# Optimization experiments

Measured on AMD Instinct MI355X. Metric: run time of the kernel, lower is better.

The kernel has to match this reference:

```python
import jax, jax.numpy as jnp
import numpy as np

QUERY_DIM = 1024
KEY_DIM = 1024
NUM_HEADS = 16
HEAD_DIM = QUERY_DIM // NUM_HEADS


def setup_inputs() -> dict:
    key = jax.random.key(0)
    ks = jax.random.split(key, 11)
    B, Sq, Sk = 2, 2048, 2048
    s = 0.02
    return {
        "q": jax.random.normal(ks[0], (B, Sq, QUERY_DIM), jnp.float32),
        "k": jax.random.normal(ks[1], (B, Sk, KEY_DIM), jnp.float32),
        "v": jax.random.normal(ks[2], (B, Sk, KEY_DIM), jnp.float32),
        "Wq": jax.random.normal(ks[3], (QUERY_DIM, QUERY_DIM), jnp.float32) * s,
        "bq": jnp.zeros((QUERY_DIM,), jnp.float32),
        "Wk": jax.random.normal(ks[4], (KEY_DIM, QUERY_DIM), jnp.float32) * s,
        "bk": jnp.zeros((QUERY_DIM,), jnp.float32),
        "Wv": jax.random.normal(ks[5], (KEY_DIM, QUERY_DIM), jnp.float32) * s,
        "bv": jnp.zeros((QUERY_DIM,), jnp.float32),
        "Wo": jax.random.normal(ks[6], (QUERY_DIM, QUERY_DIM), jnp.float32) * s,
        "bo": jnp.zeros((QUERY_DIM,), jnp.float32),
    }


def reference(q, k, v, Wq, bq, Wk, bk, Wv, bv, Wo, bo):
    B, Sq, _ = q.shape
    Sk = k.shape[1]
    scale = HEAD_DIM ** -0.5
    # projections -> [B, H, S, Dh]
    qh = (q @ Wq + bq).reshape(B, Sq, NUM_HEADS, HEAD_DIM).transpose(0, 2, 1, 3)
    kh = (k @ Wk + bk).reshape(B, Sk, NUM_HEADS, HEAD_DIM).transpose(0, 2, 1, 3)
    vh = (v @ Wv + bv).reshape(B, Sk, NUM_HEADS, HEAD_DIM).transpose(0, 2, 1, 3)
    scores = jnp.einsum("bhqd,bhkd->bhqk", qh, kh) * scale
    attn = jax.nn.softmax(scores, axis=-1)
    out = jnp.einsum("bhqk,bhkd->bhqd", attn, vh)
    out = out.transpose(0, 2, 1, 3).reshape(B, Sq, QUERY_DIM)
    return out @ Wo + bo  # dropout is identity at inference
```

## Files before the change

### kernel.cpp

```cpp
#include <hip/hip_runtime.h>
#include <hip/hip_fp16.h>
#include <cstddef>


#define B_   2
#define S_   2048
#define D_   1024
#define H_   16
#define DH_  64

typedef _Float16 half8 __attribute__((ext_vector_type(8)));
typedef _Float16 half4 __attribute__((ext_vector_type(4)));
typedef float floatx4 __attribute__((ext_vector_type(4)));

#define MFMA32(a, b, c) __builtin_amdgcn_mfma_f32_16x16x32_f16((a), (b), (c), 0, 0, 0)
#define MFMA16(a, b, c) __builtin_amdgcn_mfma_f32_16x16x16f16((a), (b), (c), 0, 0, 0)

__global__ __launch_bounds__(256) void cvt3(
    const float* __restrict__ q, const float* __restrict__ k,
    const float* __restrict__ v,
    __half* __restrict__ qf, __half* __restrict__ kf, __half* __restrict__ vf)
{
    const float* srcs[3] = {q, k, v};
    __half* dsts[3] = {qf, kf, vf};
    const int z = blockIdx.y;
    const int i = blockIdx.x * 256 + threadIdx.x;
    const float4* s = (const float4*)srcs[z];
    const float4 a = s[2 * i], b = s[2 * i + 1];
    half8 h;
    h[0] = (_Float16)a.x; h[1] = (_Float16)a.y; h[2] = (_Float16)a.z; h[3] = (_Float16)a.w;
    h[4] = (_Float16)b.x; h[5] = (_Float16)b.y; h[6] = (_Float16)b.z; h[7] = (_Float16)b.w;
    *(half8*)&dsts[z][(size_t)i * 8] = h;
}

__global__ __launch_bounds__(256) void wtrans4(
    const float* __restrict__ Wq, const float* __restrict__ Wk,
    const float* __restrict__ Wv, const float* __restrict__ Wo,
    __half* __restrict__ Wtq, __half* __restrict__ Wtk,
    __half* __restrict__ Wtv, __half* __restrict__ Wto)
{
    __shared__ __align__(16) __half T[64][72];
    const float* Ws[4] = {Wq, Wk, Wv, Wo};
    __half* Wts[4] = {Wtq, Wtk, Wtv, Wto};
    const float* W = Ws[blockIdx.z];
    __half* Wt = Wts[blockIdx.z];
    const int tid = threadIdx.x;
    const int n0 = blockIdx.x * 64, k0 = blockIdx.y * 64;
    #pragma unroll
    for (int p = 0; p < 4; ++p) {
        const int c = tid + p * 256;
        const int kr = c >> 4, nc = (c & 15) * 4;
        const float4 a = *(const float4*)&W[(size_t)(k0 + kr) * D_ + n0 + nc];
        T[nc + 0][kr] = __float2half(a.x);
        T[nc + 1][kr] = __float2half(a.y);
        T[nc + 2][kr] = __float2half(a.z);
        T[nc + 3][kr] = __float2half(a.w);
    }
    __syncthreads();
    #pragma unroll
    for (int p = 0; p < 2; ++p) {
        const int c = tid + p * 256;
        const int nr = c >> 3, kc = (c & 7) * 8;
        *(half8*)&Wt[(size_t)(n0 + nr) * D_ + k0 + kc] = *(const half8*)&T[nr][kc];
    }
}

__device__ __forceinline__ void gemm_core(
    const __half* __restrict__ A, const __half* __restrict__ Bt,
    const float* __restrict__ bias, void* __restrict__ dst,
    const int mode, const float oscale)
{
    __shared__ __align__(16) char gsm[36864];
    __half (*As)[72] = (__half(*)[72])gsm;
    __half (*Bs)[72] = (__half(*)[72])(gsm + 18432);

    const int tid = threadIdx.x;
    const int m0 = blockIdx.y * 128, n0 = blockIdx.x * 128;
    const int lane = tid & 63, wv = tid >> 6;
    const int quad = lane >> 4, lr = lane & 15;
    const int wm0 = (wv >> 1) * 64, wn0 = (wv & 1) * 64;

    floatx4 acc[4][4];
    #pragma unroll
    for (int i = 0; i < 4; ++i)
        #pragma unroll
        for (int j = 0; j < 4; ++j)
            acc[i][j] = (floatx4){0.f, 0.f, 0.f, 0.f};

    half8 pa[4], pb[4];
    #pragma unroll
    for (int p = 0; p < 4; ++p) {
        const int c = tid + p * 256;
        const int row = c >> 3, seg = (c & 7) * 8;
        pa[p] = *(const half8*)&A [(size_t)(m0 + row) * D_ + seg];
        pb[p] = *(const half8*)&Bt[(size_t)(n0 + row) * D_ + seg];
    }

    for (int k0 = 0; k0 < D_; k0 += 64) {
        __syncthreads();
        #pragma unroll
        for (int p = 0; p < 4; ++p) {
            const int c = tid + p * 256;
            const int row = c >> 3, seg = (c & 7) * 8;
            *(half8*)&As[row][seg] = pa[p];
            *(half8*)&Bs[row][seg] = pb[p];
        }
        if (k0 + 64 < D_) {
            #pragma unroll
            for (int p = 0; p < 4; ++p) {
                const int c = tid + p * 256;
                const int row = c >> 3, seg = (c & 7) * 8;
                pa[p] = *(const half8*)&A [(size_t)(m0 + row) * D_ + k0 + 64 + seg];
                pb[p] = *(const half8*)&Bt[(size_t)(n0 + row) * D_ + k0 + 64 + seg];
            }
        }
        __syncthreads();
        #pragma unroll
        for (int ks = 0; ks < 2; ++ks) {
            const int ko = quad * 8 + ks * 32;
            half8 af[4], bf[4];
            #pragma unroll
            for (int i = 0; i < 4; ++i) af[i] = *(const half8*)&As[wm0 + i * 16 + lr][ko];
            #pragma unroll
            for (int j = 0; j < 4; ++j) bf[j] = *(const half8*)&Bs[wn0 + j * 16 + lr][ko];
            #pragma unroll
            for (int i = 0; i < 4; ++i)
                #pragma unroll
                for (int j = 0; j < 4; ++j)
                    acc[i][j] = MFMA32(af[i], bf[j], acc[i][j]);
        }
    }

    if (mode == 1) {
        float* out = (float*)dst;
        #pragma unroll
        for (int i = 0; i < 4; ++i) {
            #pragma unroll
            for (int j = 0; j < 4; ++j) {
                const int col = n0 + wn0 + j * 16 + lr;
                const float bval = bias[col];
                #pragma unroll
                for (int r = 0; r < 4; ++r) {
                    const int m = m0 + wm0 + i * 16 + quad * 4 + r;
                    out[(size_t)m * D_ + col] = acc[i][j][r] + bval;
                }
            }
        }
        return;
    }

    __syncthreads();
    __half (*Ct)[136] = (__half(*)[136])gsm;
    #pragma unroll
    for (int i = 0; i < 4; ++i) {
        #pragma unroll
        for (int j = 0; j < 4; ++j) {
            const int nl = wn0 + j * 16 + lr;
            const float bval = bias[n0 + nl];
            #pragma unroll
            for (int r = 0; r < 4; ++r) {
                const int ml = wm0 + i * 16 + quad * 4 + r;
                const _Float16 hv = (_Float16)((acc[i][j][r] + bval) * oscale);
                if (mode == 0) Ct[ml][nl] = hv;
                else           Ct[nl][ml] = hv;
            }
        }
    }
    __syncthreads();
    __half* oh = (__half*)dst;
    #pragma unroll
    for (int p = 0; p < 8; ++p) {
        const int row = (tid >> 4) + p * 16;
        const int cs  = (tid & 15) * 8;
        const half8 vls = *(const half8*)&Ct[row][cs];
        if (mode == 0) {
            const int m = m0 + row, col = n0 + cs;
            const int b = m >> 11, s = m & (S_ - 1);
            const int h = col >> 6, d = col & 63;
            *(half8*)&oh[(((size_t)(b * H_ + h) * S_ + s) << 6) + d] = vls;
        } else {
            const int col = n0 + row, m = m0 + cs;
            const int b = m >> 11, s = m & (S_ - 1);
            const int h = col >> 6, d = col & 63;
            *(half8*)&oh[((size_t)(b * H_ + h) * DH_ + d) * S_ + s] = vls;
        }
    }
}

__global__ __launch_bounds__(256) void gemm_proj(
    const __half* __restrict__ qf, const __half* __restrict__ kf,
    const __half* __restrict__ vf,
    const __half* __restrict__ Wtq, const __half* __restrict__ Wtk,
    const __half* __restrict__ Wtv,
    const float* __restrict__ bq, const float* __restrict__ bk,
    const float* __restrict__ bv,
    __half* __restrict__ qhf, __half* __restrict__ khf, __half* __restrict__ vht)
{
    const __half* As[3] = {qf, kf, vf};
    const __half* Bts[3] = {Wtq, Wtk, Wtv};
    const float* bs[3] = {bq, bk, bv};
    __half* ds[3] = {qhf, khf, vht};
    const int z = blockIdx.z;
    gemm_core(As[z], Bts[z], bs[z], ds[z], z == 2 ? 2 : 0,
              z == 0 ? 0.1803368801111244f : 1.0f);
}

__global__ __launch_bounds__(256) void gemm_final(
    const __half* __restrict__ attf, const __half* __restrict__ Wto,
    const float* __restrict__ bo, float* __restrict__ out)
{
    gemm_core(attf, Wto, bo, out, 1, 1.0f);
}

__global__ __launch_bounds__(256) void attn_f16(
    const __half* __restrict__ qhf, const __half* __restrict__ khf,
    const __half* __restrict__ vht, __half* __restrict__ attf)
{
    __shared__ __align__(16) char smem[31232];
    __half (*Qs)[72] = (__half(*)[72])smem;
    __half (*Ks)[72] = (__half(*)[72])(smem + 9216);
    __half (*Vs)[72] = (__half(*)[72])(smem + 18432);

    const int tid = threadIdx.x;
    const int lane = tid & 63, wv = tid >> 6;
    const int quad = lane >> 4, lr = lane & 15;
    const int bh = blockIdx.y;
    const int q0 = blockIdx.x * 64;
    const size_t hbase = (size_t)bh * S_ * DH_;

    #pragma unroll
    for (int p = 0; p < 2; ++p) {
        const int c = tid + p * 256;
        const int row = c >> 3, seg = (c & 7) * 8;
        *(half8*)&Qs[row][seg] = *(const half8*)&qhf[hbase + (size_t)(q0 + row) * DH_ + seg];
    }
    __syncthreads();
    half8 qB[4][2];
    #pragma unroll
    for (int qs = 0; qs < 4; ++qs)
        #pragma unroll
        for (int ks = 0; ks < 2; ++ks)
            qB[qs][ks] = *(const half8*)&Qs[qs * 16 + lr][quad * 8 + ks * 32];

    float lp[4] = {0.f, 0.f, 0.f, 0.f};
    floatx4 O[4][4];
    #pragma unroll
    for (int i = 0; i < 4; ++i)
        #pragma unroll
        for (int j = 0; j < 4; ++j)
            O[i][j] = (floatx4){0.f, 0.f, 0.f, 0.f};

    half8 pk[2], pv[2];
    #pragma unroll
    for (int p = 0; p < 2; ++p) {
        const int c = tid + p * 256;
        const int row = c >> 3, seg = (c & 7) * 8;
        pk[p] = *(const half8*)&khf[hbase + (size_t)row * DH_ + seg];
        pv[p] = *(const half8*)&vht[hbase + (size_t)row * S_ + seg];
    }

    for (int kt = 0; kt < S_; kt += 64) {
        __syncthreads();
        #pragma unroll
        for (int p = 0; p < 2; ++p) {
            const int c = tid + p * 256;
            const int row = c >> 3, seg = (c & 7) * 8;
            *(half8*)&Ks[row][seg] = pk[p];
            *(half8*)&Vs[row][seg] = pv[p];
        }
        if (kt + 64 < S_) {
            #pragma unroll
            for (int p = 0; p < 2; ++p) {
                const int c = tid + p * 256;
                const int row = c >> 3, seg = (c & 7) * 8;
                pk[p] = *(const half8*)&khf[hbase + (size_t)(kt + 64 + row) * DH_ + seg];
                pv[p] = *(const half8*)&vht[hbase + (size_t)row * S_ + kt + 64 + seg];
            }
        }
        __syncthreads();

        floatx4 s4[4];
        #pragma unroll
        for (int qs = 0; qs < 4; ++qs) s4[qs] = (floatx4){0.f, 0.f, 0.f, 0.f};
        #pragma unroll
        for (int ks = 0; ks < 2; ++ks) {
            const half8 aK = *(const half8*)&Ks[wv * 16 + lr][quad * 8 + ks * 32];
            #pragma unroll
            for (int qs = 0; qs < 4; ++qs)
                s4[qs] = MFMA32(aK, qB[qs][ks], s4[qs]);
        }

        half4 pB[4];
        #pragma unroll
        for (int qs = 0; qs < 4; ++qs) {
            #pragma unroll
            for (int r = 0; r < 4; ++r) {
                const float p = __builtin_amdgcn_exp2f(s4[qs][r]);
                lp[qs] += p;
                pB[qs][r] = (_Float16)p;
            }
        }

        #pragma unroll
        for (int ds = 0; ds < 4; ++ds) {
            const half4 aV = *(const half4*)&Vs[ds * 16 + lr][wv * 16 + quad * 4];
            #pragma unroll
            for (int qs = 0; qs < 4; ++qs)
                O[ds][qs] = MFMA16(aV, pB[qs], O[ds][qs]);
        }
    }

    __syncthreads();
    float* L    = (float*)(smem + 17408);
    float* invL = (float*)(smem + 21504);
    float (*R)[68] = (float(*)[68])smem;
    __half (*F)[72] = (__half(*)[72])(smem + 22016);

    #pragma unroll
    for (int qs = 0; qs < 4; ++qs)
        L[(wv * 4 + quad) * 64 + qs * 16 + lr] = lp[qs];
    __syncthreads();
    if (tid < 64) {
        float s = 0.f;
        #pragma unroll
        for (int i = 0; i < 16; ++i) s += L[i * 64 + tid];
        invL[tid] = 1.0f / s;
    }
    __syncthreads();

    const int qc = tid & 63, dg = tid >> 6;
    const float il = invL[qc];

    #pragma unroll
    for (int ds = 0; ds < 4; ++ds) {
        __syncthreads();
        #pragma unroll
        for (int qs = 0; qs < 4; ++qs)
            #pragma unroll
            for (int r = 0; r < 4; ++r)
                R[wv * 16 + quad * 4 + r][qs * 16 + lr] = O[ds][qs][r];
        __syncthreads();
        half4 hv;
        #pragma unroll
        for (int rr = 0; rr < 4; ++rr) {
            const int row = dg * 4 + rr;
            const float v = R[row][qc] + R[16 + row][qc] + R[32 + row][qc] + R[48 + row][qc];
            hv[rr] = (_Float16)(v * il);
        }
        *(half4*)&F[qc][ds * 16 + dg * 4] = hv;
    }
    __syncthreads();

    const int b = bh >> 4, h = bh & 15;
    const int qrow = tid >> 2, dseg = (tid & 3) * 16;
    __half* dstp = &attf[(((size_t)(b * S_ + q0 + qrow)) << 10) + h * DH_ + dseg];
    *(half8*)&dstp[0] = *(const half8*)&F[qrow][dseg];
    *(half8*)&dstp[8] = *(const half8*)&F[qrow][dseg + 8];
}

extern "C" void kernel_launch(void* const* d_in, const int* in_sizes, int n_in,
                              void* d_out, int out_size, void* d_ws, size_t ws_size,
                              hipStream_t stream) {
    const float* q  = (const float*)d_in[0];
    const float* k  = (const float*)d_in[1];
    const float* v  = (const float*)d_in[2];
    const float* Wq = (const float*)d_in[3];
    const float* bq = (const float*)d_in[4];
    const float* Wk = (const float*)d_in[5];
    const float* bk = (const float*)d_in[6];
    const float* Wv = (const float*)d_in[7];
    const float* bv = (const float*)d_in[8];
    const float* Wo = (const float*)d_in[9];
    const float* bo = (const float*)d_in[10];
    float* out = (float*)d_out;

    __half* ws = (__half*)d_ws;
    const size_t NE = (size_t)B_ * S_ * D_;
    __half* qf   = ws;
    __half* kf   = ws + NE;
    __half* vf   = ws + 2 * NE;
    __half* qhf  = ws + 3 * NE;
    __half* khf  = ws + 4 * NE;
    __half* vht  = ws + 5 * NE;
    __half* attf = ws + 6 * NE;
    __half* Wtq  = ws + 7 * NE;
    __half* Wtk  = Wtq + (size_t)D_ * D_;
    __half* Wtv  = Wtk + (size_t)D_ * D_;
    __half* Wto  = Wtv + (size_t)D_ * D_;

    const dim3 blk(256);
    cvt3<<<dim3((unsigned)(NE / 8 / 256), 3), blk, 0, stream>>>(q, k, v, qf, kf, vf);
    wtrans4<<<dim3(16, 16, 4), blk, 0, stream>>>(Wq, Wk, Wv, Wo, Wtq, Wtk, Wtv, Wto);

    gemm_proj<<<dim3(D_ / 128, (B_ * S_) / 128, 3), blk, 0, stream>>>(
        qf, kf, vf, Wtq, Wtk, Wtv, bq, bk, bv, qhf, khf, vht);

    attn_f16<<<dim3(S_ / 64, B_ * H_), blk, 0, stream>>>(qhf, khf, vht, attf);

    gemm_final<<<dim3(D_ / 128, (B_ * S_) / 128), blk, 0, stream>>>(attf, Wto, bo, out);
}
```

Baseline: 232.5 us.

## Load K/V fragments directly into registers in attention; merge prep kernels

The attention loop stops staging K and V tiles through shared memory. Each lane now loads its MFMA operand fragments straight from global memory, with the next K fragment prefetched into registers, which removes the per-tile LDS writes and both block barriers. Separately, the fp16 conversion and weight-transpose kernels are merged into one launch with a flat grid to cut launch overhead. The cost is that each lane issues narrower, less coalesced global loads (the V loads are 8-byte strided rows), and there is no shared reuse across waves, so more L2 traffic is risked.

```diff
diff --git a/kernel.cpp b/kernel.cpp
--- a/kernel.cpp
+++ b/kernel.cpp
@@ -16,36 +16,38 @@
 #define MFMA32(a, b, c) __builtin_amdgcn_mfma_f32_16x16x32_f16((a), (b), (c), 0, 0, 0)
 #define MFMA16(a, b, c) __builtin_amdgcn_mfma_f32_16x16x16f16((a), (b), (c), 0, 0, 0)
 
-__global__ __launch_bounds__(256) void cvt3(
+__global__ __launch_bounds__(256) void prep(
     const float* __restrict__ q, const float* __restrict__ k,
     const float* __restrict__ v,
-    __half* __restrict__ qf, __half* __restrict__ kf, __half* __restrict__ vf)
-{
-    const float* srcs[3] = {q, k, v};
-    __half* dsts[3] = {qf, kf, vf};
-    const int z = blockIdx.y;
-    const int i = blockIdx.x * 256 + threadIdx.x;
-    const float4* s = (const float4*)srcs[z];
-    const float4 a = s[2 * i], b = s[2 * i + 1];
-    half8 h;
-    h[0] = (_Float16)a.x; h[1] = (_Float16)a.y; h[2] = (_Float16)a.z; h[3] = (_Float16)a.w;
-    h[4] = (_Float16)b.x; h[5] = (_Float16)b.y; h[6] = (_Float16)b.z; h[7] = (_Float16)b.w;
-    *(half8*)&dsts[z][(size_t)i * 8] = h;
-}
-
-__global__ __launch_bounds__(256) void wtrans4(
+    __half* __restrict__ qf, __half* __restrict__ kf, __half* __restrict__ vf,
     const float* __restrict__ Wq, const float* __restrict__ Wk,
     const float* __restrict__ Wv, const float* __restrict__ Wo,
     __half* __restrict__ Wtq, __half* __restrict__ Wtk,
     __half* __restrict__ Wtv, __half* __restrict__ Wto)
 {
     __shared__ __align__(16) __half T[64][72];
+    const int tid = threadIdx.x;
+    const int bz = blockIdx.x;
+    if (bz < 6144) {
+        const float* srcs[3] = {q, k, v};
+        __half* dsts[3] = {qf, kf, vf};
+        const int z = bz >> 11;
+        const int i = (bz & 2047) * 256 + tid;
+        const float4* s = (const float4*)srcs[z];
+        const float4 a = s[2 * i], b = s[2 * i + 1];
+        half8 h;
+        h[0] = (_Float16)a.x; h[1] = (_Float16)a.y; h[2] = (_Float16)a.z; h[3] = (_Float16)a.w;
+        h[4] = (_Float16)b.x; h[5] = (_Float16)b.y; h[6] = (_Float16)b.z; h[7] = (_Float16)b.w;
+        *(half8*)&dsts[z][(size_t)i * 8] = h;
+        return;
+    }
+    const int idx = bz - 6144;
     const float* Ws[4] = {Wq, Wk, Wv, Wo};
     __half* Wts[4] = {Wtq, Wtk, Wtv, Wto};
-    const float* W = Ws[blockIdx.z];
-    __half* Wt = Wts[blockIdx.z];
-    const int tid = threadIdx.x;
-    const int n0 = blockIdx.x * 64, k0 = blockIdx.y * 64;
+    const float* W = Ws[idx >> 8];
+    __half* Wt = Wts[idx >> 8];
+    const int r = idx & 255;
+    const int n0 = (r & 15) * 64, k0 = (r >> 4) * 64;
     #pragma unroll
     for (int p = 0; p < 4; ++p) {
         const int c = tid + p * 256;
@@ -218,8 +220,6 @@
 {
     __shared__ __align__(16) char smem[31232];
     __half (*Qs)[72] = (__half(*)[72])smem;
-    __half (*Ks)[72] = (__half(*)[72])(smem + 9216);
-    __half (*Vs)[72] = (__half(*)[72])(smem + 18432);
 
     const int tid = threadIdx.x;
     const int lane = tid & 63, wv = tid >> 6;
@@ -241,6 +241,7 @@
         #pragma unroll
         for (int ks = 0; ks < 2; ++ks)
             qB[qs][ks] = *(const half8*)&Qs[qs * 16 + lr][quad * 8 + ks * 32];
+    __syncthreads();
 
     float lp[4] = {0.f, 0.f, 0.f, 0.f};
     floatx4 O[4][4];
@@ -250,45 +251,32 @@
         for (int j = 0; j < 4; ++j)
             O[i][j] = (floatx4){0.f, 0.f, 0.f, 0.f};
 
-    half8 pk[2], pv[2];
-    #pragma unroll
-    for (int p = 0; p < 2; ++p) {
-        const int c = tid + p * 256;
-        const int row = c >> 3, seg = (c & 7) * 8;
-        pk[p] = *(const half8*)&khf[hbase + (size_t)row * DH_ + seg];
-        pv[p] = *(const half8*)&vht[hbase + (size_t)row * S_ + seg];
-    }
+    const __half* kp = khf + hbase + (size_t)(wv * 16 + lr) * DH_ + quad * 8;
+    const __half* vp = vht + hbase + (size_t)lr * S_ + wv * 16 + quad * 4;
+
+    half8 cK0 = *(const half8*)(kp);
+    half8 cK1 = *(const half8*)(kp + 32);
 
     for (int kt = 0; kt < S_; kt += 64) {
-        __syncthreads();
-        #pragma unroll
-        for (int p = 0; p < 2; ++p) {
-            const int c = tid + p * 256;
-            const int row = c >> 3, seg = (c & 7) * 8;
-            *(half8*)&Ks[row][seg] = pk[p];
-            *(half8*)&Vs[row][seg] = pv[p];
-        }
+        half4 cV[4];
+        #pragma unroll
+        for (int ds = 0; ds < 4; ++ds)
+            cV[ds] = *(const half4*)(vp + (size_t)ds * 16 * S_ + kt);
+
+        half8 nK0, nK1;
         if (kt + 64 < S_) {
-            #pragma unroll
-            for (int p = 0; p < 2; ++p) {
-                const int c = tid + p * 256;
-                const int row = c >> 3, seg = (c & 7) * 8;
-                pk[p] = *(const half8*)&khf[hbase + (size_t)(kt + 64 + row) * DH_ + seg];
-                pv[p] = *(const half8*)&vht[hbase + (size_t)row * S_ + kt + 64 + seg];
-            }
-        }
-        __syncthreads();
+            const __half* kn = kp + (size_t)(kt + 64) * DH_;
+            nK0 = *(const half8*)(kn);
+            nK1 = *(const half8*)(kn + 32);
+        }
 
         floatx4 s4[4];
         #pragma unroll
         for (int qs = 0; qs < 4; ++qs) s4[qs] = (floatx4){0.f, 0.f, 0.f, 0.f};
         #pragma unroll
-        for (int ks = 0; ks < 2; ++ks) {
-            const half8 aK = *(const half8*)&Ks[wv * 16 + lr][quad * 8 + ks * 32];
-            #pragma unroll
-            for (int qs = 0; qs < 4; ++qs)
-                s4[qs] = MFMA32(aK, qB[qs][ks], s4[qs]);
-        }
+        for (int qs = 0; qs < 4; ++qs) s4[qs] = MFMA32(cK0, qB[qs][0], s4[qs]);
+        #pragma unroll
+        for (int qs = 0; qs < 4; ++qs) s4[qs] = MFMA32(cK1, qB[qs][1], s4[qs]);
 
         half4 pB[4];
         #pragma unroll
@@ -303,14 +291,14 @@
 
         #pragma unroll
         for (int ds = 0; ds < 4; ++ds) {
-            const half4 aV = *(const half4*)&Vs[ds * 16 + lr][wv * 16 + quad * 4];
             #pragma unroll
             for (int qs = 0; qs < 4; ++qs)
-                O[ds][qs] = MFMA16(aV, pB[qs], O[ds][qs]);
-        }
-    }
-
-    __syncthreads();
+                O[ds][qs] = MFMA16(cV[ds], pB[qs], O[ds][qs]);
+        }
+
+        cK0 = nK0; cK1 = nK1;
+    }
+
     float* L    = (float*)(smem + 17408);
     float* invL = (float*)(smem + 21504);
     float (*R)[68] = (float(*)[68])smem;
@@ -389,8 +377,8 @@
     __half* Wto  = Wtv + (size_t)D_ * D_;
 
     const dim3 blk(256);
-    cvt3<<<dim3((unsigned)(NE / 8 / 256), 3), blk, 0, stream>>>(q, k, v, qf, kf, vf);
-    wtrans4<<<dim3(16, 16, 4), blk, 0, stream>>>(Wq, Wk, Wv, Wo, Wtq, Wtk, Wtv, Wto);
+    prep<<<dim3(7168), blk, 0, stream>>>(q, k, v, qf, kf, vf,
+                                         Wq, Wk, Wv, Wo, Wtq, Wtk, Wtv, Wto);
 
     gemm_proj<<<dim3(D_ / 128, (B_ * S_) / 128, 3), blk, 0, stream>>>(
         qf, kf, vf, Wtq, Wtk, Wtv, bq, bk, bv, qhf, khf, vht);
```

Result: slower. 294.9 us (+26.9%).

## Swizzle GEMM block order and widen attention key tiles to 128

Applied to the files above, without the earlier changes.

Adds a grouped block-index swizzle to the projection and output GEMMs so neighbouring blocks share A/B tiles in cache. The attention kernel now processes 128 keys per iteration instead of 64, with each wave handling two 16-key groups. This halves the number of barrier-synchronised load/compute iterations and the per-tile overhead. The cost is more shared memory, with the K buffer aliased onto the Q staging area, which needs an extra sync, plus more prefetch registers.

```diff
diff --git a/kernel.cpp b/kernel.cpp
--- a/kernel.cpp
+++ b/kernel.cpp
@@ -68,14 +68,13 @@
 __device__ __forceinline__ void gemm_core(
     const __half* __restrict__ A, const __half* __restrict__ Bt,
     const float* __restrict__ bias, void* __restrict__ dst,
-    const int mode, const float oscale)
+    const int mode, const float oscale, const int m0, const int n0)
 {
     __shared__ __align__(16) char gsm[36864];
     __half (*As)[72] = (__half(*)[72])gsm;
     __half (*Bs)[72] = (__half(*)[72])(gsm + 18432);
 
     const int tid = threadIdx.x;
-    const int m0 = blockIdx.y * 128, n0 = blockIdx.x * 128;
     const int lane = tid & 63, wv = tid >> 6;
     const int quad = lane >> 4, lr = lane & 15;
     const int wm0 = (wv >> 1) * 64, wn0 = (wv & 1) * 64;
@@ -187,6 +186,13 @@
     }
 }
 
+__device__ __forceinline__ void swizzle_mn(int& m0, int& n0) {
+    const int id = blockIdx.y * gridDim.x + blockIdx.x;
+    const int grp = id >> 5, within = id & 31;
+    m0 = (grp * 4 + (within & 3)) * 128;
+    n0 = (within >> 2) * 128;
+}
+
 __global__ __launch_bounds__(256) void gemm_proj(
     const __half* __restrict__ qf, const __half* __restrict__ kf,
     const __half* __restrict__ vf,
@@ -201,25 +207,27 @@
     const float* bs[3] = {bq, bk, bv};
     __half* ds[3] = {qhf, khf, vht};
     const int z = blockIdx.z;
+    int m0, n0; swizzle_mn(m0, n0);
     gemm_core(As[z], Bts[z], bs[z], ds[z], z == 2 ? 2 : 0,
-              z == 0 ? 0.1803368801111244f : 1.0f);
+              z == 0 ? 0.1803368801111244f : 1.0f, m0, n0);
 }
 
 __global__ __launch_bounds__(256) void gemm_final(
     const __half* __restrict__ attf, const __half* __restrict__ Wto,
     const float* __restrict__ bo, float* __restrict__ out)
 {
-    gemm_core(attf, Wto, bo, out, 1, 1.0f);
+    int m0, n0; swizzle_mn(m0, n0);
+    gemm_core(attf, Wto, bo, out, 1, 1.0f, m0, n0);
 }
 
 __global__ __launch_bounds__(256) void attn_f16(
     const __half* __restrict__ qhf, const __half* __restrict__ khf,
     const __half* __restrict__ vht, __half* __restrict__ attf)
 {
-    __shared__ __align__(16) char smem[31232];
-    __half (*Qs)[72] = (__half(*)[72])smem;
-    __half (*Ks)[72] = (__half(*)[72])(smem + 9216);
-    __half (*Vs)[72] = (__half(*)[72])(smem + 18432);
+    __shared__ __align__(16) char smem[35840];
+    __half (*Ks)[72]  = (__half(*)[72])smem;
+    __half (*Vs)[136] = (__half(*)[136])(smem + 18432);
+    __half (*Qs)[72]  = (__half(*)[72])smem;
 
     const int tid = threadIdx.x;
     const int lane = tid & 63, wv = tid >> 6;
@@ -241,6 +249,7 @@
         #pragma unroll
         for (int ks = 0; ks < 2; ++ks)
             qB[qs][ks] = *(const half8*)&Qs[qs * 16 + lr][quad * 8 + ks * 32];
+    __syncthreads();
 
     float lp[4] = {0.f, 0.f, 0.f, 0.f};
     floatx4 O[4][4];
@@ -250,63 +259,70 @@
         for (int j = 0; j < 4; ++j)
             O[i][j] = (floatx4){0.f, 0.f, 0.f, 0.f};
 
-    half8 pk[2], pv[2];
-    #pragma unroll
-    for (int p = 0; p < 2; ++p) {
+    half8 pk[4], pv[4];
+    #pragma unroll
+    for (int p = 0; p < 4; ++p) {
         const int c = tid + p * 256;
-        const int row = c >> 3, seg = (c & 7) * 8;
-        pk[p] = *(const half8*)&khf[hbase + (size_t)row * DH_ + seg];
-        pv[p] = *(const half8*)&vht[hbase + (size_t)row * S_ + seg];
-    }
-
-    for (int kt = 0; kt < S_; kt += 64) {
-        __syncthreads();
-        #pragma unroll
-        for (int p = 0; p < 2; ++p) {
+        const int krow = c >> 3, kseg = (c & 7) * 8;
+        const int vrow = c >> 4, vseg = (c & 15) * 8;
+        pk[p] = *(const half8*)&khf[hbase + (size_t)krow * DH_ + kseg];
+        pv[p] = *(const half8*)&vht[hbase + (size_t)vrow * S_ + vseg];
+    }
+
+    for (int kt = 0; kt < S_; kt += 128) {
+        __syncthreads();
+        #pragma unroll
+        for (int p = 0; p < 4; ++p) {
             const int c = tid + p * 256;
-            const int row = c >> 3, seg = (c & 7) * 8;
-            *(half8*)&Ks[row][seg] = pk[p];
-            *(half8*)&Vs[row][seg] = pv[p];
-        }
-        if (kt + 64 < S_) {
-            #pragma unroll
-            for (int p = 0; p < 2; ++p) {
+            const int krow = c >> 3, kseg = (c & 7) * 8;
+            const int vrow = c >> 4, vseg = (c & 15) * 8;
+            *(half8*)&Ks[krow][kseg] = pk[p];
+            *(half8*)&Vs[vrow][vseg] = pv[p];
+        }
+        if (kt + 128 < S_) {
+            #pragma unroll
+            for (int p = 0; p < 4; ++p) {
                 const int c = tid + p * 256;
-                const int row = c >> 3, seg = (c & 7) * 8;
-                pk[p] = *(const half8*)&khf[hbase + (size_t)(kt + 64 + row) * DH_ + seg];
-                pv[p] = *(const half8*)&vht[hbase + (size_t)row * S_ + kt + 64 + seg];
-            }
-        }
-        __syncthreads();
-
-        floatx4 s4[4];
-        #pragma unroll
-        for (int qs = 0; qs < 4; ++qs) s4[qs] = (floatx4){0.f, 0.f, 0.f, 0.f};
-        #pragma unroll
-        for (int ks = 0; ks < 2; ++ks) {
-            const half8 aK = *(const half8*)&Ks[wv * 16 + lr][quad * 8 + ks * 32];
-            #pragma unroll
-            for (int qs = 0; qs < 4; ++qs)
-                s4[qs] = MFMA32(aK, qB[qs][ks], s4[qs]);
-        }
-
-        half4 pB[4];
-        #pragma unroll
-        for (int qs = 0; qs < 4; ++qs) {
-            #pragma unroll
-            for (int r = 0; r < 4; ++r) {
-                const float p = __builtin_amdgcn_exp2f(s4[qs][r]);
-                lp[qs] += p;
-                pB[qs][r] = (_Float16)p;
-            }
-        }
-
-        #pragma unroll
-        for (int ds = 0; ds < 4; ++ds) {
-            const half4 aV = *(const half4*)&Vs[ds * 16 + lr][wv * 16 + quad * 4];
-            #pragma unroll
-            for (int qs = 0; qs < 4; ++qs)
-                O[ds][qs] = MFMA16(aV, pB[qs], O[ds][qs]);
+                const int krow = c >> 3, kseg = (c & 7) * 8;
+                const int vrow = c >> 4, vseg = (c & 15) * 8;
+                pk[p] = *(const half8*)&khf[hbase + (size_t)(kt + 128 + krow) * DH_ + kseg];
+                pv[p] = *(const half8*)&vht[hbase + (size_t)vrow * S_ + kt + 128 + vseg];
+            }
+        }
+        __syncthreads();
+
+        #pragma unroll
+        for (int g = 0; g < 2; ++g) {
+            const int kr = wv * 32 + g * 16 + lr;
+            const half8 aK0 = *(const half8*)&Ks[kr][quad * 8];
+            const half8 aK1 = *(const half8*)&Ks[kr][quad * 8 + 32];
+
+            floatx4 s4[4];
+            #pragma unroll
+            for (int qs = 0; qs < 4; ++qs) s4[qs] = (floatx4){0.f, 0.f, 0.f, 0.f};
+            #pragma unroll
+            for (int qs = 0; qs < 4; ++qs) s4[qs] = MFMA32(aK0, qB[qs][0], s4[qs]);
+            #pragma unroll
+            for (int qs = 0; qs < 4; ++qs) s4[qs] = MFMA32(aK1, qB[qs][1], s4[qs]);
+
+            half4 pB[4];
+            #pragma unroll
+            for (int qs = 0; qs < 4; ++qs) {
+                #pragma unroll
+                for (int r = 0; r < 4; ++r) {
+                    const float p = __builtin_amdgcn_exp2f(s4[qs][r]);
+                    lp[qs] += p;
+                    pB[qs][r] = (_Float16)p;
+                }
+            }
+
+            #pragma unroll
+            for (int ds = 0; ds < 4; ++ds) {
+                const half4 aV = *(const half4*)&Vs[ds * 16 + lr][wv * 32 + g * 16 + quad * 4];
+                #pragma unroll
+                for (int qs = 0; qs < 4; ++qs)
+                    O[ds][qs] = MFMA16(aV, pB[qs], O[ds][qs]);
+            }
         }
     }
 
```

After: 234.1 us. No clear change (+0.7%).

## Double-buffer attention K/V tiles, MFMA row sums, merge prep kernels

Applied to the files above, without the earlier changes.

Merges the fp16 conversion and weight-transpose kernels into a single launch. In the attention kernel, K/V tiles are double-buffered in shared memory, which leaves one barrier per iteration instead of two. Softmax row sums are now computed with an MFMA against a ones vector rather than scalar adds, which simplifies the final reduction. The cost is more LDS per block (36 KB), which may lower occupancy.

```diff
diff --git a/kernel.cpp b/kernel.cpp
--- a/kernel.cpp
+++ b/kernel.cpp
@@ -16,36 +16,38 @@
 #define MFMA32(a, b, c) __builtin_amdgcn_mfma_f32_16x16x32_f16((a), (b), (c), 0, 0, 0)
 #define MFMA16(a, b, c) __builtin_amdgcn_mfma_f32_16x16x16f16((a), (b), (c), 0, 0, 0)
 
-__global__ __launch_bounds__(256) void cvt3(
+__global__ __launch_bounds__(256) void prep(
     const float* __restrict__ q, const float* __restrict__ k,
     const float* __restrict__ v,
-    __half* __restrict__ qf, __half* __restrict__ kf, __half* __restrict__ vf)
-{
-    const float* srcs[3] = {q, k, v};
-    __half* dsts[3] = {qf, kf, vf};
-    const int z = blockIdx.y;
-    const int i = blockIdx.x * 256 + threadIdx.x;
-    const float4* s = (const float4*)srcs[z];
-    const float4 a = s[2 * i], b = s[2 * i + 1];
-    half8 h;
-    h[0] = (_Float16)a.x; h[1] = (_Float16)a.y; h[2] = (_Float16)a.z; h[3] = (_Float16)a.w;
-    h[4] = (_Float16)b.x; h[5] = (_Float16)b.y; h[6] = (_Float16)b.z; h[7] = (_Float16)b.w;
-    *(half8*)&dsts[z][(size_t)i * 8] = h;
-}
-
-__global__ __launch_bounds__(256) void wtrans4(
+    __half* __restrict__ qf, __half* __restrict__ kf, __half* __restrict__ vf,
     const float* __restrict__ Wq, const float* __restrict__ Wk,
     const float* __restrict__ Wv, const float* __restrict__ Wo,
     __half* __restrict__ Wtq, __half* __restrict__ Wtk,
     __half* __restrict__ Wtv, __half* __restrict__ Wto)
 {
     __shared__ __align__(16) __half T[64][72];
+    const int tid = threadIdx.x;
+    const int bz = blockIdx.x;
+    if (bz < 6144) {
+        const float* srcs[3] = {q, k, v};
+        __half* dsts[3] = {qf, kf, vf};
+        const int z = bz >> 11;
+        const int i = (bz & 2047) * 256 + tid;
+        const float4* s = (const float4*)srcs[z];
+        const float4 a = s[2 * i], b = s[2 * i + 1];
+        half8 h;
+        h[0] = (_Float16)a.x; h[1] = (_Float16)a.y; h[2] = (_Float16)a.z; h[3] = (_Float16)a.w;
+        h[4] = (_Float16)b.x; h[5] = (_Float16)b.y; h[6] = (_Float16)b.z; h[7] = (_Float16)b.w;
+        *(half8*)&dsts[z][(size_t)i * 8] = h;
+        return;
+    }
+    const int idx = bz - 6144;
     const float* Ws[4] = {Wq, Wk, Wv, Wo};
     __half* Wts[4] = {Wtq, Wtk, Wtv, Wto};
-    const float* W = Ws[blockIdx.z];
-    __half* Wt = Wts[blockIdx.z];
-    const int tid = threadIdx.x;
-    const int n0 = blockIdx.x * 64, k0 = blockIdx.y * 64;
+    const float* W = Ws[idx >> 8];
+    __half* Wt = Wts[idx >> 8];
+    const int r = idx & 255;
+    const int n0 = (r & 15) * 64, k0 = (r >> 4) * 64;
     #pragma unroll
     for (int p = 0; p < 4; ++p) {
         const int c = tid + p * 256;
@@ -216,10 +218,8 @@
     const __half* __restrict__ qhf, const __half* __restrict__ khf,
     const __half* __restrict__ vht, __half* __restrict__ attf)
 {
-    __shared__ __align__(16) char smem[31232];
+    __shared__ __align__(16) char smem[36864];
     __half (*Qs)[72] = (__half(*)[72])smem;
-    __half (*Ks)[72] = (__half(*)[72])(smem + 9216);
-    __half (*Vs)[72] = (__half(*)[72])(smem + 18432);
 
     const int tid = threadIdx.x;
     const int lane = tid & 63, wv = tid >> 6;
@@ -241,89 +241,113 @@
         #pragma unroll
         for (int ks = 0; ks < 2; ++ks)
             qB[qs][ks] = *(const half8*)&Qs[qs * 16 + lr][quad * 8 + ks * 32];
-
-    float lp[4] = {0.f, 0.f, 0.f, 0.f};
+    __syncthreads();
+
     floatx4 O[4][4];
     #pragma unroll
     for (int i = 0; i < 4; ++i)
         #pragma unroll
         for (int j = 0; j < 4; ++j)
             O[i][j] = (floatx4){0.f, 0.f, 0.f, 0.f};
-
-    half8 pk[2], pv[2];
-    #pragma unroll
-    for (int p = 0; p < 2; ++p) {
-        const int c = tid + p * 256;
-        const int row = c >> 3, seg = (c & 7) * 8;
-        pk[p] = *(const half8*)&khf[hbase + (size_t)row * DH_ + seg];
-        pv[p] = *(const half8*)&vht[hbase + (size_t)row * S_ + seg];
-    }
-
-    for (int kt = 0; kt < S_; kt += 64) {
-        __syncthreads();
+    floatx4 sums[4] = {{0.f,0.f,0.f,0.f},{0.f,0.f,0.f,0.f},
+                       {0.f,0.f,0.f,0.f},{0.f,0.f,0.f,0.f}};
+    const half4 ones = {(_Float16)1.f, (_Float16)1.f, (_Float16)1.f, (_Float16)1.f};
+
+    {
+        half8 pk[2], pv[2];
         #pragma unroll
         for (int p = 0; p < 2; ++p) {
             const int c = tid + p * 256;
             const int row = c >> 3, seg = (c & 7) * 8;
-            *(half8*)&Ks[row][seg] = pk[p];
-            *(half8*)&Vs[row][seg] = pv[p];
-        }
-        if (kt + 64 < S_) {
+            pk[p] = *(const half8*)&khf[hbase + (size_t)row * DH_ + seg];
+            pv[p] = *(const half8*)&vht[hbase + (size_t)row * S_ + seg];
+        }
+        __half (*Ks0)[72] = (__half(*)[72])smem;
+        __half (*Vs0)[72] = (__half(*)[72])(smem + 18432);
+        #pragma unroll
+        for (int p = 0; p < 2; ++p) {
+            const int c = tid + p * 256;
+            const int row = c >> 3, seg = (c & 7) * 8;
+            *(half8*)&Ks0[row][seg] = pk[p];
+            *(half8*)&Vs0[row][seg] = pv[p];
+        }
+    }
+    __syncthreads();
+
+    for (int it = 0; it < 32; ++it) {
+        const int buf = it & 1;
+        const int ktn = (it + 1) * 64;
+        __half (*Ksb)[72] = (__half(*)[72])(smem + buf * 9216);
+        __half (*Vsb)[72] = (__half(*)[72])(smem + 18432 + buf * 9216);
+
+        half8 nk[2], nv[2];
+        if (ktn < S_) {
             #pragma unroll
             for (int p = 0; p < 2; ++p) {
                 const int c = tid + p * 256;
                 const int row = c >> 3, seg = (c & 7) * 8;
-                pk[p] = *(const half8*)&khf[hbase + (size_t)(kt + 64 + row) * DH_ + seg];
-                pv[p] = *(const half8*)&vht[hbase + (size_t)row * S_ + kt + 64 + seg];
+                nk[p] = *(const half8*)&khf[hbase + (size_t)(ktn + row) * DH_ + seg];
+                nv[p] = *(const half8*)&vht[hbase + (size_t)row * S_ + ktn + seg];
             }
         }
-        __syncthreads();
 
         floatx4 s4[4];
         #pragma unroll
         for (int qs = 0; qs < 4; ++qs) s4[qs] = (floatx4){0.f, 0.f, 0.f, 0.f};
-        #pragma unroll
-        for (int ks = 0; ks < 2; ++ks) {
-            const half8 aK = *(const half8*)&Ks[wv * 16 + lr][quad * 8 + ks * 32];
-            #pragma unroll
-            for (int qs = 0; qs < 4; ++qs)
-                s4[qs] = MFMA32(aK, qB[qs][ks], s4[qs]);
-        }
+        const half8 aK0 = *(const half8*)&Ksb[wv * 16 + lr][quad * 8];
+        const half8 aK1 = *(const half8*)&Ksb[wv * 16 + lr][quad * 8 + 32];
+        #pragma unroll
+        for (int qs = 0; qs < 4; ++qs) s4[qs] = MFMA32(aK0, qB[qs][0], s4[qs]);
+        #pragma unroll
+        for (int qs = 0; qs < 4; ++qs) s4[qs] = MFMA32(aK1, qB[qs][1], s4[qs]);
 
         half4 pB[4];
         #pragma unroll
         for (int qs = 0; qs < 4; ++qs) {
             #pragma unroll
-            for (int r = 0; r < 4; ++r) {
-                const float p = __builtin_amdgcn_exp2f(s4[qs][r]);
-                lp[qs] += p;
-                pB[qs][r] = (_Float16)p;
-            }
-        }
+            for (int r = 0; r < 4; ++r)
+                pB[qs][r] = (_Float16)__builtin_amdgcn_exp2f(s4[qs][r]);
+        }
+
+        #pragma unroll
+        for (int qs = 0; qs < 4; ++qs)
+            sums[qs] = MFMA16(ones, pB[qs], sums[qs]);
 
         #pragma unroll
         for (int ds = 0; ds < 4; ++ds) {
-            const half4 aV = *(const half4*)&Vs[ds * 16 + lr][wv * 16 + quad * 4];
+            const half4 aV = *(const half4*)&Vsb[ds * 16 + lr][wv * 16 + quad * 4];
             #pragma unroll
             for (int qs = 0; qs < 4; ++qs)
                 O[ds][qs] = MFMA16(aV, pB[qs], O[ds][qs]);
         }
-    }
-
-    __syncthreads();
+
+        if (ktn < S_) {
+            __half (*Ksn)[72] = (__half(*)[72])(smem + (buf ^ 1) * 9216);
+            __half (*Vsn)[72] = (__half(*)[72])(smem + 18432 + (buf ^ 1) * 9216);
+            #pragma unroll
+            for (int p = 0; p < 2; ++p) {
+                const int c = tid + p * 256;
+                const int row = c >> 3, seg = (c & 7) * 8;
+                *(half8*)&Ksn[row][seg] = nk[p];
+                *(half8*)&Vsn[row][seg] = nv[p];
+            }
+        }
+        __syncthreads();
+    }
+
+    float (*R)[68] = (float(*)[68])smem;
     float* L    = (float*)(smem + 17408);
-    float* invL = (float*)(smem + 21504);
-    float (*R)[68] = (float(*)[68])smem;
+    float* invL = (float*)(smem + 18432);
     __half (*F)[72] = (__half(*)[72])(smem + 22016);
 
-    #pragma unroll
-    for (int qs = 0; qs < 4; ++qs)
-        L[(wv * 4 + quad) * 64 + qs * 16 + lr] = lp[qs];
+    if (quad == 0) {
+        #pragma unroll
+        for (int qs = 0; qs < 4; ++qs)
+            L[wv * 64 + qs * 16 + lr] = sums[qs][0];
+    }
     __syncthreads();
     if (tid < 64) {
-        float s = 0.f;
-        #pragma unroll
-        for (int i = 0; i < 16; ++i) s += L[i * 64 + tid];
+        const float s = L[tid] + L[64 + tid] + L[128 + tid] + L[192 + tid];
         invL[tid] = 1.0f / s;
     }
     __syncthreads();
@@ -389,8 +413,8 @@
     __half* Wto  = Wtv + (size_t)D_ * D_;
 
     const dim3 blk(256);
-    cvt3<<<dim3((unsigned)(NE / 8 / 256), 3), blk, 0, stream>>>(q, k, v, qf, kf, vf);
-    wtrans4<<<dim3(16, 16, 4), blk, 0, stream>>>(Wq, Wk, Wv, Wo, Wtq, Wtk, Wtv, Wto);
+    prep<<<dim3(7168), blk, 0, stream>>>(q, k, v, qf, kf, vf,
+                                         Wq, Wk, Wv, Wo, Wtq, Wtk, Wtv, Wto);
 
     gemm_proj<<<dim3(D_ / 128, (B_ * S_) / 128, 3), blk, 0, stream>>>(
         qf, kf, vf, Wtq, Wtk, Wtv, bq, bk, bv, qhf, khf, vht);
```

New measurement: 248.9 us. 1.07x slower.
